# Kernel optimization log

Hardware: AMD Instinct MI355X
Metric: run time of the kernel (lower is better)

## Reference

```python
import jax, jax.numpy as jnp
import numpy as np

N, E, G, T, H, ED, IN_D, OUT_D = 50000, 1600000, 64, 5, 64, 9, 10, 3
EPS = 1e-6

def _seg_mean(vals, seg, num):
    s = jax.ops.segment_sum(vals, seg, num_segments=num)
    c = jax.ops.segment_sum(jnp.ones((vals.shape[0],), vals.dtype), seg, num_segments=num)
    return s / jnp.maximum(c, 1.0)[:, None], c

def per_graph_edge_norm(edge_attr, edge_graph, num_graphs):
    # standardize each edge-feature column per graph (zero-shot transfer trick)
    mu, _ = _seg_mean(edge_attr, edge_graph, num_graphs)
    sq, _ = _seg_mean(edge_attr * edge_attr, edge_graph, num_graphs)
    var = jnp.maximum(sq - mu * mu, 0.0)
    std = jnp.sqrt(var)
    return (edge_attr - mu[edge_graph]) / (std[edge_graph] + EPS)

def setup_inputs() -> dict:
    key = jax.random.key(0)
    ks = jax.random.split(key, 24)
    s = 0.05  # weight scale to keep ReLU chains stable
    inp = {
        'x': jax.random.normal(ks[0], (N, IN_D), jnp.float32),
        'edge_index': jax.random.randint(ks[1], (2, E), 0, N),
        'edge_attr': jax.random.normal(ks[2], (E, ED), jnp.float32),
        'batch': jnp.sort(jax.random.randint(ks[3], (N,), 0, G)),
        'lift_W1': jax.random.normal(ks[4], (IN_D, H), jnp.float32) * s,
        'lift_b1': jnp.zeros((H,), jnp.float32),
        'lift_W2': jax.random.normal(ks[5], (H, H), jnp.float32) * s,
        'lift_b2': jnp.zeros((H,), jnp.float32),
        'Wself': jax.random.normal(ks[6], (T, H, H), jnp.float32) * s,
        'bself': jnp.zeros((T, H), jnp.float32),
        'msg_W0': jax.random.normal(ks[7], (T, H + ED, H), jnp.float32) * s,
        'msg_b0': jnp.zeros((T, H), jnp.float32),
        'msg_W1': jax.random.normal(ks[8], (T, H, H), jnp.float32) * s,
        'msg_b1': jnp.zeros((T, H), jnp.float32),
        'msg_W2': jax.random.normal(ks[9], (T, H, H), jnp.float32) * s,
        'msg_b2': jnp.zeros((T, H), jnp.float32),
        'gate_W': jax.random.normal(ks[10], (T, 1, H), jnp.float32) * s,
        'gate_b': jnp.zeros((T, H), jnp.float32),
        'proj_W1': jax.random.normal(ks[11], (H, H), jnp.float32) * s,
        'proj_b1': jnp.zeros((H,), jnp.float32),
        'proj_W2': jax.random.normal(ks[12], (H, OUT_D), jnp.float32) * s,
        'proj_b2': jnp.zeros((OUT_D,), jnp.float32),
    }
    return inp

def _gno(x, edge_index, edge_attr, batch,
         lift_W1, lift_b1, lift_W2, lift_b2,
         Wself, bself, msg_W0, msg_b0, msg_W1, msg_b1, msg_W2, msg_b2,
         gate_W, gate_b, proj_W1, proj_b1, proj_W2, proj_b2):
    src, dst = edge_index[0], edge_index[1]
    edge_graph = batch[src]
    ea = per_graph_edge_norm(edge_attr, edge_graph, G)  # cols 0:9 == all cols
    log_diag_y = x[:, 4:5]                               # [N,1]
    v0 = jax.nn.relu(x @ lift_W1 + lift_b1) @ lift_W2 + lift_b2  # lift
    v = v0
    for t in range(T):
        # gather -> per-edge MLP -> scatter-mean (AdmittanceKernelLayer)
        h = jnp.concatenate([v[src], ea], axis=-1)              # [E, H+ED]
        h = jax.nn.relu(h @ msg_W0[t] + msg_b0[t])
        h = jax.nn.relu(h @ msg_W1[t] + msg_b1[t])
        m = h @ msg_W2[t] + msg_b2[t]                           # [E, H]
        agg, _ = _seg_mean(m, dst, N)                           # mean aggregation
        gate = jax.nn.sigmoid(log_diag_y @ gate_W[t] + gate_b[t])  # [N,H]
        v = jax.nn.relu(v @ Wself[t] + bself[t] + agg + v0) * gate
        # dropout inactive at inference
    out = jax.nn.relu(v @ proj_W1 + proj_b1) @ proj_W2 + proj_b2  # project
    return out

def reference(x, edge_index, edge_attr, batch,
              lift_W1, lift_b1, lift_W2, lift_b2,
              Wself, bself, msg_W0, msg_b0, msg_W1, msg_b1, msg_W2, msg_b2,
              gate_W, gate_b, proj_W1, proj_b1, proj_W2, proj_b2):
    return _gno(x, edge_index, edge_attr, batch,
                lift_W1, lift_b1, lift_W2, lift_b2,
                Wself, bself, msg_W0, msg_b0, msg_W1, msg_b1, msg_W2, msg_b2,
                gate_W, gate_b, proj_W1, proj_b1, proj_W2, proj_b2)
```

## Files before the change

### kernel.cpp

```cpp
#include <hip/hip_runtime.h>
#include <math.h>

#define NN 50000
#define NE 1600000
#define NG 64
#define NT 5
#define NH 64
#define NED 9
#define NIN 10
#define NOUT 3
#define EPSF 1e-6f
#define NSUB (NE / 16)
#define STATS_BLKS 2048
#define STATS_SLICE (2 * NG * NED + NG)

typedef __attribute__((ext_vector_type(8))) short s8v;
typedef __attribute__((ext_vector_type(4))) short s4v;
typedef __attribute__((ext_vector_type(4))) float f32x4;

__device__ __forceinline__ unsigned short f2bf(float f) {
    union { float f; unsigned int u; } v; v.f = f;
    unsigned int r = v.u + 0x7FFFu + ((v.u >> 16) & 1u);
    return (unsigned short)(r >> 16);
}
__device__ __forceinline__ float bf2f(unsigned short b) {
    union { unsigned int u; float f; } v; v.u = ((unsigned int)b) << 16;
    return v.f;
}

__global__ __launch_bounds__(256) void stats_kernel(
    const int* __restrict__ ei, const float* __restrict__ ea,
    const int* __restrict__ batch,
    float* __restrict__ blockAcc, int* __restrict__ ecnt) {
    __shared__ float lsum[NG * NED];
    __shared__ float lsq[NG * NED];
    __shared__ float lcnt[NG];
    for (int i = threadIdx.x; i < NG * NED; i += blockDim.x) { lsum[i] = 0.f; lsq[i] = 0.f; }
    for (int i = threadIdx.x; i < NG; i += blockDim.x) lcnt[i] = 0.f;
    __syncthreads();
    const int TOT = NE * NED;
    int stride = gridDim.x * blockDim.x;
    for (int i = blockIdx.x * blockDim.x + threadIdx.x; i < TOT; i += stride) {
        int e = (int)(((unsigned long long)i * 0x1C71C71D) >> 32);
        int d = i - e * NED;
        float a = ea[i];
        int g = batch[ei[e]];
        atomicAdd(&lsum[g * NED + d], a);
        atomicAdd(&lsq[g * NED + d], a * a);
        if (d == 0) {
            atomicAdd(&lcnt[g], 1.0f);
            atomicAdd(&ecnt[ei[NE + e]], 1);
        }
    }
    __syncthreads();
    float* dst = blockAcc + (size_t)blockIdx.x * STATS_SLICE;
    for (int i = threadIdx.x; i < NG * NED; i += blockDim.x) {
        dst[i] = lsum[i];
        dst[NG * NED + i] = lsq[i];
    }
    for (int i = threadIdx.x; i < NG; i += blockDim.x) dst[2 * NG * NED + i] = lcnt[i];
}

__global__ void stats_merge(const float* __restrict__ blockAcc,
                            float* __restrict__ ssum, float* __restrict__ ssq,
                            float* __restrict__ scnt) {
    int i = blockIdx.x * 256 + threadIdx.x;
    if (i >= STATS_SLICE) return;
    float a = 0.f;
    for (int b = 0; b < STATS_BLKS; ++b) a += blockAcc[(size_t)b * STATS_SLICE + i];
    if (i < NG * NED) ssum[i] = a;
    else if (i < 2 * NG * NED) ssq[i - NG * NED] = a;
    else scnt[i - 2 * NG * NED] = a;
}

__global__ void stats_fin(const float* __restrict__ ssum, const float* __restrict__ ssq,
                          const float* __restrict__ scnt,
                          float* __restrict__ mu, float* __restrict__ rstd) {
    int i = blockIdx.x * blockDim.x + threadIdx.x;
    if (i >= NG * NED) return;
    int g = i / NED;
    float c = fmaxf(scnt[g], 1.0f);
    float m = ssum[i] / c;
    float q = ssq[i] / c;
    float var = fmaxf(q - m * m, 0.f);
    mu[i] = m;
    rstd[i] = 1.0f / (sqrtf(var) + EPSF);
}

__global__ void scan1_kernel(const int* __restrict__ ecnt, int* __restrict__ partial) {
    __shared__ int sm[256];
    int i = blockIdx.x * 256 + threadIdx.x;
    sm[threadIdx.x] = (i < NN) ? ecnt[i] : 0;
    __syncthreads();
    for (int off = 128; off; off >>= 1) {
        if (threadIdx.x < off) sm[threadIdx.x] += sm[threadIdx.x + off];
        __syncthreads();
    }
    if (threadIdx.x == 0) partial[blockIdx.x] = sm[0];
}
__global__ void scan2_kernel(int* __restrict__ partial, int nb) {
    __shared__ int sm[256];
    int t = threadIdx.x;
    sm[t] = (t < nb) ? partial[t] : 0;
    __syncthreads();
    for (int off = 1; off < 256; off <<= 1) {
        int v = (t >= off) ? sm[t - off] : 0;
        __syncthreads();
        sm[t] += v;
        __syncthreads();
    }
    if (t < nb) partial[t] = (t ? sm[t - 1] : 0);
}
__global__ void scan3_kernel(const int* __restrict__ ecnt, const int* __restrict__ partial,
                             int* __restrict__ offs) {
    __shared__ int sm[256];
    int b = blockIdx.x, t = threadIdx.x, i = b * 256 + t;
    int x = (i < NN) ? ecnt[i] : 0;
    sm[t] = x;
    __syncthreads();
    for (int off = 1; off < 256; off <<= 1) {
        int v = (t >= off) ? sm[t - off] : 0;
        __syncthreads();
        sm[t] += v;
        __syncthreads();
    }
    if (i < NN) offs[i] = sm[t] - x + partial[b];
}

__global__ void permute_kernel(const int* __restrict__ ei, const int* __restrict__ offs,
                               int* __restrict__ cursor, int* __restrict__ perm) {
    int stride = gridDim.x * blockDim.x;
    for (int e = blockIdx.x * blockDim.x + threadIdx.x; e < NE; e += stride) {
        int d = ei[NE + e];
        int pos = offs[d] + atomicAdd(&cursor[d], 1);
        perm[pos] = e;
    }
}

__global__ void pack_kernel(const int* __restrict__ perm, const int* __restrict__ ei,
                            const float* __restrict__ ea, const int* __restrict__ batch,
                            const float* __restrict__ mu, const float* __restrict__ rstd,
                            int* __restrict__ srcPerm, int* __restrict__ dstPerm,
                            unsigned short* __restrict__ eaN) {
    int stride = gridDim.x * blockDim.x;
    for (int p = blockIdx.x * blockDim.x + threadIdx.x; p < NE; p += stride) {
        int e = perm[p];
        int s = ei[e], d = ei[NE + e];
        int g = batch[s];
        srcPerm[p] = s;
        dstPerm[p] = d;
#pragma unroll
        for (int k = 0; k < NED; ++k) {
            float val = (ea[(size_t)e * NED + k] - mu[g * NED + k]) * rstd[g * NED + k];
            eaN[(size_t)k * NE + p] = f2bf(val);
        }
    }
}

__global__ __launch_bounds__(256) void lift_kernel(
    const float* __restrict__ x,
    const float* __restrict__ W1, const float* __restrict__ b1,
    const float* __restrict__ W2, const float* __restrict__ b2,
    float* __restrict__ v0, float* __restrict__ v, float* __restrict__ ldy) {
    __shared__ float sW1[NIN * NH];
    __shared__ __align__(16) float sW2[NH][NH];
    __shared__ float sb1[NH], sb2[NH];
    for (int i = threadIdx.x; i < NIN * NH; i += blockDim.x) sW1[i] = W1[i];
    for (int i = threadIdx.x; i < NH * NH; i += blockDim.x) {
        int k = i >> 6, j = i & 63;
        sW2[j][k] = W2[i];
    }
    for (int i = threadIdx.x; i < NH; i += blockDim.x) { sb1[i] = b1[i]; sb2[i] = b2[i]; }
    __syncthreads();
    int stride = gridDim.x * blockDim.x;
    for (int n = blockIdx.x * blockDim.x + threadIdx.x; n < NN; n += stride) {
        float xr[NIN];
#pragma unroll
        for (int k = 0; k < NIN; ++k) xr[k] = x[(size_t)n * NIN + k];
        ldy[n] = xr[4];
        float h[NH];
#pragma unroll
        for (int j = 0; j < NH; ++j) {
            float acc = sb1[j];
#pragma unroll
            for (int k = 0; k < NIN; ++k) acc += xr[k] * sW1[k * NH + j];
            h[j] = fmaxf(acc, 0.f);
        }
#pragma unroll
        for (int j = 0; j < NH; ++j) {
            float acc = sb2[j];
#pragma unroll
            for (int k = 0; k < NH; k += 4) {
                float4 w = *(const float4*)&sW2[j][k];
                acc += h[k] * w.x + h[k + 1] * w.y + h[k + 2] * w.z + h[k + 3] * w.w;
            }
            v0[(size_t)n * NH + j] = acc;
            v[(size_t)n * NH + j] = acc;
        }
    }
}

__device__ __forceinline__ void gemm_acc68(const float* __restrict__ Ab,
                                           const float* __restrict__ Wb,
                                           int K, int te, int tj, float acc[4][4]) {
#pragma unroll 4
    for (int k = 0; k < K; ++k) {
        float4 a = *(const float4*)(Ab + k * 68 + (te << 2));
        float4 b = *(const float4*)(Wb + (k << 6) + (tj << 2));
        acc[0][0] = fmaf(a.x, b.x, acc[0][0]);
        acc[0][1] = fmaf(a.x, b.y, acc[0][1]);
        acc[0][2] = fmaf(a.x, b.z, acc[0][2]);
        acc[0][3] = fmaf(a.x, b.w, acc[0][3]);
        acc[1][0] = fmaf(a.y, b.x, acc[1][0]);
        acc[1][1] = fmaf(a.y, b.y, acc[1][1]);
        acc[1][2] = fmaf(a.y, b.z, acc[1][2]);
        acc[1][3] = fmaf(a.y, b.w, acc[1][3]);
        acc[2][0] = fmaf(a.z, b.x, acc[2][0]);
        acc[2][1] = fmaf(a.z, b.y, acc[2][1]);
        acc[2][2] = fmaf(a.z, b.z, acc[2][2]);
        acc[2][3] = fmaf(a.z, b.w, acc[2][3]);
        acc[3][0] = fmaf(a.w, b.x, acc[3][0]);
        acc[3][1] = fmaf(a.w, b.y, acc[3][1]);
        acc[3][2] = fmaf(a.w, b.z, acc[3][2]);
        acc[3][3] = fmaf(a.w, b.w, acc[3][3]);
    }
}

__global__ __launch_bounds__(256, 4) void u_kernel(
    const float* __restrict__ v, const float* __restrict__ W0v,
    const float* __restrict__ b0, unsigned short* __restrict__ Ubf) {
    __shared__ __align__(16) float Vt[64][68];
    __shared__ __align__(16) float sW[64][64];
    __shared__ float sb[64];
    const int tid = threadIdx.x;
    const int base = blockIdx.x * 64;
    const int te = tid >> 4, tj = tid & 15;

    {
        int r = tid >> 2;
        int kb = (tid & 3) << 4;
        int n = base + r;
        const float4* vrow = (const float4*)(v + (size_t)n * NH + kb);
#pragma unroll
        for (int q = 0; q < 4; ++q) {
            float4 f = (n < NN) ? vrow[q] : make_float4(0.f, 0.f, 0.f, 0.f);
            int k = kb + q * 4;
            Vt[k + 0][r] = f.x; Vt[k + 1][r] = f.y; Vt[k + 2][r] = f.z; Vt[k + 3][r] = f.w;
        }
    }
    for (int i4 = tid; i4 < 64 * 16; i4 += 256) {
        int k = i4 >> 4, c4 = i4 & 15;
        *(float4*)&sW[k][c4 * 4] = *(const float4*)(W0v + (size_t)k * 64 + c4 * 4);
    }
    if (tid < 64) sb[tid] = b0[tid];
    __syncthreads();

    float acc[4][4];
    {
        float b0_ = sb[tj * 4 + 0], b1_ = sb[tj * 4 + 1], b2_ = sb[tj * 4 + 2], b3_ = sb[tj * 4 + 3];
#pragma unroll
        for (int ee = 0; ee < 4; ++ee) { acc[ee][0] = b0_; acc[ee][1] = b1_; acc[ee][2] = b2_; acc[ee][3] = b3_; }
    }
    gemm_acc68(&Vt[0][0], &sW[0][0], 64, te, tj, acc);

#pragma unroll
    for (int ee = 0; ee < 4; ++ee) {
        int n = base + te * 4 + ee;
        if (n < NN) {
            s4v p;
            p[0] = (short)f2bf(acc[ee][0]);
            p[1] = (short)f2bf(acc[ee][1]);
            p[2] = (short)f2bf(acc[ee][2]);
            p[3] = (short)f2bf(acc[ee][3]);
            *(s4v*)&Ubf[(size_t)n * NH + tj * 4] = p;
        }
    }
}

__global__ __launch_bounds__(256, 4) void edge4_kernel(
    const int* __restrict__ srcPerm, const int* __restrict__ dstPerm,
    const unsigned short* __restrict__ eaN,
    const float* __restrict__ W0e, const float* __restrict__ W1, const float* __restrict__ b1,
    const unsigned short* __restrict__ Ubf, float* __restrict__ nodesum) {
    __shared__ __align__(16) float sWe[NED][64];
    __shared__ __align__(16) short W1frag[8][64][8];
    __shared__ __align__(16) short h0bf[4][16 * 64];
    __shared__ __align__(16) float h1s[4][16 * 64];
    __shared__ int sDstS[4][16];

    const int tid = threadIdx.x;
    const int lane = tid & 63, w = tid >> 6;
    const int l15 = lane & 15, l4 = lane >> 4;

    for (int i4 = tid; i4 < NED * 16; i4 += 256) {
        int k = i4 >> 4, c4 = i4 & 15;
        *(float4*)&sWe[k][c4 * 4] = *(const float4*)(W0e + (size_t)k * 64 + c4 * 4);
    }
    for (int idx = tid; idx < 2 * 4 * 64; idx += 256) {
        int kc = idx >> 8, c = (idx >> 6) & 3, ln = idx & 63;
        int fl15 = ln & 15, fl4 = ln >> 4;
        int col = 16 * c + fl15;
        s8v frag;
#pragma unroll
        for (int j = 0; j < 8; ++j) {
            int k = kc * 32 + fl4 * 8 + j;
            frag[j] = (short)f2bf(W1[(size_t)k * 64 + col]);
        }
        *(s8v*)&W1frag[kc * 4 + c][ln][0] = frag;
    }
    float b1r[4];
#pragma unroll
    for (int c = 0; c < 4; ++c) b1r[c] = b1[16 * c + l15];
    __syncthreads();

    short* myh0 = h0bf[w];
    float* myh1 = h1s[w];
    int*   myd  = sDstS[w];
    const int gw = blockIdx.x * 4 + w;
    const int nw = gridDim.x * 4;

    for (int st = gw; st < NSUB; st += nw) {
        const int e16 = st * 16;
        if (lane < 16) myd[lane] = dstPerm[e16 + lane];

        int4 s4 = *(const int4*)(srcPerm + e16 + 4 * l4);
        ushort4 eu[NED];
#pragma unroll
        for (int d = 0; d < NED; ++d)
            eu[d] = *(const ushort4*)(eaN + (size_t)d * NE + e16 + 4 * l4);

        float acc0[4][4];
        {
            const int* sp = (const int*)&s4;
#pragma unroll
            for (int ee = 0; ee < 4; ++ee) {
                s4v u4 = *(const s4v*)(Ubf + (size_t)sp[ee] * NH + 4 * l15);
                acc0[ee][0] = bf2f((unsigned short)u4[0]);
                acc0[ee][1] = bf2f((unsigned short)u4[1]);
                acc0[ee][2] = bf2f((unsigned short)u4[2]);
                acc0[ee][3] = bf2f((unsigned short)u4[3]);
            }
        }
#pragma unroll
        for (int d = 0; d < NED; ++d) {
            float4 wv = *(const float4*)&sWe[d][4 * l15];
            float a0 = bf2f((unsigned short)eu[d].x), a1 = bf2f((unsigned short)eu[d].y);
            float a2 = bf2f((unsigned short)eu[d].z), a3 = bf2f((unsigned short)eu[d].w);
            acc0[0][0] = fmaf(a0, wv.x, acc0[0][0]); acc0[0][1] = fmaf(a0, wv.y, acc0[0][1]);
            acc0[0][2] = fmaf(a0, wv.z, acc0[0][2]); acc0[0][3] = fmaf(a0, wv.w, acc0[0][3]);
            acc0[1][0] = fmaf(a1, wv.x, acc0[1][0]); acc0[1][1] = fmaf(a1, wv.y, acc0[1][1]);
            acc0[1][2] = fmaf(a1, wv.z, acc0[1][2]); acc0[1][3] = fmaf(a1, wv.w, acc0[1][3]);
            acc0[2][0] = fmaf(a2, wv.x, acc0[2][0]); acc0[2][1] = fmaf(a2, wv.y, acc0[2][1]);
            acc0[2][2] = fmaf(a2, wv.z, acc0[2][2]); acc0[2][3] = fmaf(a2, wv.w, acc0[2][3]);
            acc0[3][0] = fmaf(a3, wv.x, acc0[3][0]); acc0[3][1] = fmaf(a3, wv.y, acc0[3][1]);
            acc0[3][2] = fmaf(a3, wv.z, acc0[3][2]); acc0[3][3] = fmaf(a3, wv.w, acc0[3][3]);
        }

#pragma unroll
        for (int ee = 0; ee < 4; ++ee) {
            int row = 4 * l4 + ee;
            s4v p;
            p[0] = (short)f2bf(fmaxf(acc0[ee][0], 0.f));
            p[1] = (short)f2bf(fmaxf(acc0[ee][1], 0.f));
            p[2] = (short)f2bf(fmaxf(acc0[ee][2], 0.f));
            p[3] = (short)f2bf(fmaxf(acc0[ee][3], 0.f));
            *(s4v*)((char*)myh0 + row * 128 + ((l15 * 8) ^ ((row & 7) << 4))) = p;
        }

        f32x4 acc[4];
#pragma unroll
        for (int c = 0; c < 4; ++c) {
            float b = b1r[c];
            acc[c][0] = b; acc[c][1] = b; acc[c][2] = b; acc[c][3] = b;
        }
        {
            const char* abase = (const char*)myh0 + l15 * 128;
            const int aswz = (l15 & 7) << 4;
#pragma unroll
            for (int kc = 0; kc < 2; ++kc) {
                s8v af = *(const s8v*)(abase + ((l4 * 16 + kc * 64) ^ aswz));
#pragma unroll
                for (int c = 0; c < 4; ++c) {
                    s8v bf = *(const s8v*)&W1frag[kc * 4 + c][lane][0];
                    acc[c] = __builtin_amdgcn_mfma_f32_16x16x32_bf16(af, bf, acc[c], 0, 0, 0);
                }
            }
        }

        int dFirst = myd[0];
        int dLast = myd[15];
        if (dFirst == dLast) {
#pragma unroll
            for (int c = 0; c < 4; ++c) {
                float vs = fmaxf(acc[c][0], 0.f) + fmaxf(acc[c][1], 0.f) +
                           fmaxf(acc[c][2], 0.f) + fmaxf(acc[c][3], 0.f);
                vs += __shfl_xor(vs, 16);
                vs += __shfl_xor(vs, 32);
                if (l4 == 0)
                    atomicAdd(&nodesum[(size_t)dFirst * NH + 16 * c + l15], vs);
            }
        } else {
#pragma unroll
            for (int r = 0; r < 4; ++r) {
                int row = 4 * l4 + r;
#pragma unroll
                for (int c = 0; c < 4; ++c)
                    myh1[row * 64 + ((16 * c + l15) ^ (l4 * 8))] = fmaxf(acc[c][r], 0.f);
            }
            int cur = dFirst;
            float a = myh1[lane];
#pragma unroll
            for (int i = 1; i < 16; ++i) {
                int dn = myd[i];
                float hv = myh1[i * 64 + (lane ^ ((i >> 2) * 8))];
                if (dn != cur) {
                    atomicAdd(&nodesum[(size_t)cur * NH + lane], a);
                    cur = dn;
                    a = hv;
                } else {
                    a += hv;
                }
            }
            atomicAdd(&nodesum[(size_t)cur * NH + lane], a);
        }
    }
}

__global__ __launch_bounds__(256, 2) void update3_kernel(
    const float* __restrict__ Wself, const float* __restrict__ bself,
    const float* __restrict__ W2, const float* __restrict__ b2,
    const float* __restrict__ gWt, const float* __restrict__ gbt,
    const float* __restrict__ v0, const float* __restrict__ ldy,
    const int* __restrict__ ecnt, float* __restrict__ nodesum,
    float* __restrict__ v) {
    __shared__ __align__(16) float Vt[64][68];
    __shared__ __align__(16) float St[64][68];
    __shared__ __align__(16) float sWs[64][64];
    __shared__ __align__(16) float sW2[64][64];
    __shared__ float sbs[64], sb2[64], sgw[64], sgb[64];
    const int tid = threadIdx.x;
    const int base = blockIdx.x * 64;
    const int te = tid >> 4, tj = tid & 15;

    {
        int r = tid >> 2;
        int kb = (tid & 3) << 4;
        int n = base + r;
        const float4* vrow = (const float4*)(v + (size_t)n * NH + kb);
        float4* srow = (float4*)(nodesum + (size_t)n * NH + kb);
        const float4 z4 = make_float4(0.f, 0.f, 0.f, 0.f);
#pragma unroll
        for (int q = 0; q < 4; ++q) {
            float4 f = (n < NN) ? vrow[q] : z4;
            float4 g = (n < NN) ? srow[q] : z4;
            if (n < NN) srow[q] = z4;
            int k = kb + q * 4;
            Vt[k + 0][r] = f.x; Vt[k + 1][r] = f.y; Vt[k + 2][r] = f.z; Vt[k + 3][r] = f.w;
            St[k + 0][r] = g.x; St[k + 1][r] = g.y; St[k + 2][r] = g.z; St[k + 3][r] = g.w;
        }
    }
    for (int i4 = tid; i4 < 64 * 16; i4 += 256) {
        int k = i4 >> 4, c4 = i4 & 15;
        *(float4*)&sWs[k][c4 * 4] = *(const float4*)(Wself + (size_t)k * 64 + c4 * 4);
        *(float4*)&sW2[k][c4 * 4] = *(const float4*)(W2 + (size_t)k * 64 + c4 * 4);
    }
    if (tid < 64) { sbs[tid] = bself[tid]; sb2[tid] = b2[tid]; sgw[tid] = gWt[tid]; sgb[tid] = gbt[tid]; }
    __syncthreads();

    float acc1[4][4], acc2[4][4];
    {
        float b0_ = sbs[tj * 4 + 0], b1_ = sbs[tj * 4 + 1], b2_ = sbs[tj * 4 + 2], b3_ = sbs[tj * 4 + 3];
#pragma unroll
        for (int ee = 0; ee < 4; ++ee) {
            acc1[ee][0] = b0_; acc1[ee][1] = b1_; acc1[ee][2] = b2_; acc1[ee][3] = b3_;
            acc2[ee][0] = 0.f; acc2[ee][1] = 0.f; acc2[ee][2] = 0.f; acc2[ee][3] = 0.f;
        }
    }
    gemm_acc68(&Vt[0][0], &sWs[0][0], 64, te, tj, acc1);
    gemm_acc68(&St[0][0], &sW2[0][0], 64, te, tj, acc2);

    float gw0 = sgw[tj * 4 + 0], gw1 = sgw[tj * 4 + 1], gw2 = sgw[tj * 4 + 2], gw3 = sgw[tj * 4 + 3];
    float gb0 = sgb[tj * 4 + 0], gb1 = sgb[tj * 4 + 1], gb2 = sgb[tj * 4 + 2], gb3 = sgb[tj * 4 + 3];
    float bb0 = sb2[tj * 4 + 0], bb1 = sb2[tj * 4 + 1], bb2 = sb2[tj * 4 + 2], bb3 = sb2[tj * 4 + 3];
#pragma unroll
    for (int ee = 0; ee < 4; ++ee) {
        int n = base + te * 4 + ee;
        if (n >= NN) continue;
        float cnt = (float)ecnt[n];
        float has = (cnt > 0.5f) ? 1.f : 0.f;
        float dninv = has / fmaxf(cnt, 1.f);
        float ld = ldy[n];
        float4 v0r = *(const float4*)&v0[(size_t)n * NH + tj * 4];
        float z0 = acc1[ee][0] + acc2[ee][0] * dninv + bb0 * has + v0r.x;
        float z1 = acc1[ee][1] + acc2[ee][1] * dninv + bb1 * has + v0r.y;
        float z2 = acc1[ee][2] + acc2[ee][2] * dninv + bb2 * has + v0r.z;
        float z3 = acc1[ee][3] + acc2[ee][3] * dninv + bb3 * has + v0r.w;
        float g0 = 1.f / (1.f + expf(-(ld * gw0 + gb0)));
        float g1 = 1.f / (1.f + expf(-(ld * gw1 + gb1)));
        float g2 = 1.f / (1.f + expf(-(ld * gw2 + gb2)));
        float g3 = 1.f / (1.f + expf(-(ld * gw3 + gb3)));
        *(float4*)&v[(size_t)n * NH + tj * 4] =
            make_float4(fmaxf(z0, 0.f) * g0, fmaxf(z1, 0.f) * g1,
                        fmaxf(z2, 0.f) * g2, fmaxf(z3, 0.f) * g3);
    }
}

__global__ __launch_bounds__(256) void proj_kernel(
    const float* __restrict__ v,
    const float* __restrict__ pW1, const float* __restrict__ pb1,
    const float* __restrict__ pW2, const float* __restrict__ pb2,
    float* __restrict__ out) {
    __shared__ __align__(16) float sW1[NH][NH];
    __shared__ float sb1[NH];
    __shared__ float sW2[NH * NOUT];
    __shared__ float sb2[NOUT];
    for (int i = threadIdx.x; i < NH * NH; i += blockDim.x) {
        int k = i >> 6, j = i & 63;
        sW1[j][k] = pW1[i];
    }
    for (int i = threadIdx.x; i < NH; i += blockDim.x) sb1[i] = pb1[i];
    for (int i = threadIdx.x; i < NH * NOUT; i += blockDim.x) sW2[i] = pW2[i];
    for (int i = threadIdx.x; i < NOUT; i += blockDim.x) sb2[i] = pb2[i];
    __syncthreads();
    int stride = gridDim.x * blockDim.x;
    for (int n = blockIdx.x * blockDim.x + threadIdx.x; n < NN; n += stride) {
        float vr[NH];
        const float4* vp = (const float4*)(v + (size_t)n * NH);
#pragma unroll
        for (int q = 0; q < NH / 4; ++q) {
            float4 f = vp[q];
            vr[4 * q + 0] = f.x; vr[4 * q + 1] = f.y; vr[4 * q + 2] = f.z; vr[4 * q + 3] = f.w;
        }
        float o0 = sb2[0], o1 = sb2[1], o2 = sb2[2];
#pragma unroll
        for (int j = 0; j < NH; ++j) {
            float acc = sb1[j];
#pragma unroll
            for (int k = 0; k < NH; k += 4) {
                float4 w = *(const float4*)&sW1[j][k];
                acc += vr[k] * w.x + vr[k + 1] * w.y + vr[k + 2] * w.z + vr[k + 3] * w.w;
            }
            float h = fmaxf(acc, 0.f);
            o0 += h * sW2[j * NOUT + 0];
            o1 += h * sW2[j * NOUT + 1];
            o2 += h * sW2[j * NOUT + 2];
        }
        out[(size_t)n * NOUT + 0] = o0;
        out[(size_t)n * NOUT + 1] = o1;
        out[(size_t)n * NOUT + 2] = o2;
    }
}

extern "C" void kernel_launch(void* const* d_in, const int* in_sizes, int n_in,
                              void* d_out, int out_size, void* d_ws, size_t ws_size,
                              hipStream_t stream) {
    (void)in_sizes; (void)n_in; (void)out_size; (void)ws_size;
    const float* x     = (const float*)d_in[0];
    const int*   ei    = (const int*)d_in[1];
    const float* ea    = (const float*)d_in[2];
    const int*   batch = (const int*)d_in[3];
    const float* lW1   = (const float*)d_in[4];
    const float* lb1   = (const float*)d_in[5];
    const float* lW2   = (const float*)d_in[6];
    const float* lb2   = (const float*)d_in[7];
    const float* Wself = (const float*)d_in[8];
    const float* bself = (const float*)d_in[9];
    const float* mW0   = (const float*)d_in[10];
    const float* mb0   = (const float*)d_in[11];
    const float* mW1   = (const float*)d_in[12];
    const float* mb1   = (const float*)d_in[13];
    const float* mW2   = (const float*)d_in[14];
    const float* mb2   = (const float*)d_in[15];
    const float* gW    = (const float*)d_in[16];
    const float* gb    = (const float*)d_in[17];
    const float* pW1   = (const float*)d_in[18];
    const float* pb1   = (const float*)d_in[19];
    const float* pW2   = (const float*)d_in[20];
    const float* pb2   = (const float*)d_in[21];
    float* out = (float*)d_out;
    float* ws  = (float*)d_ws;

    float* nodesum = ws;
    float* v0   = nodesum + (size_t)NN * NH;
    float* v    = v0 + (size_t)NN * NH;
    unsigned short* Ubf = (unsigned short*)(v + (size_t)NN * NH);
    float* ldy  = (float*)Ubf + (size_t)NN * NH;
    float* mu   = ldy + NN;
    float* rstd = mu + NG * NED;
    float* ssum = rstd + NG * NED;
    float* ssq  = ssum + NG * NED;
    float* scnt = ssq + NG * NED;
    int*   ecnt   = (int*)(scnt + NG);
    int*   cursor = ecnt + NN;
    int*   offs    = cursor + NN;
    int*   partial = offs + NN;
    int*   srcPerm = partial + 256;
    int*   dstPerm = srcPerm + NE;
    unsigned short* eaN = (unsigned short*)(dstPerm + NE);
    float* statsPart = (float*)(eaN + (size_t)NED * NE);
    int*   perm = (int*)nodesum;

    const int NBLK = (NN + 63) / 64;
    const int SBLK = (NN + 255) / 256;

    hipMemsetAsync(ecnt, 0, (size_t)2 * NN * sizeof(int), stream);

    stats_kernel<<<STATS_BLKS, 256, 0, stream>>>(ei, ea, batch, statsPart, ecnt);
    stats_merge<<<(STATS_SLICE + 255) / 256, 256, 0, stream>>>(statsPart, ssum, ssq, scnt);
    stats_fin<<<3, 256, 0, stream>>>(ssum, ssq, scnt, mu, rstd);
    scan1_kernel<<<SBLK, 256, 0, stream>>>(ecnt, partial);
    scan2_kernel<<<1, 256, 0, stream>>>(partial, SBLK);
    scan3_kernel<<<SBLK, 256, 0, stream>>>(ecnt, partial, offs);
    permute_kernel<<<2048, 256, 0, stream>>>(ei, offs, cursor, perm);
    pack_kernel<<<2048, 256, 0, stream>>>(perm, ei, ea, batch, mu, rstd, srcPerm, dstPerm, eaN);
    lift_kernel<<<200, 256, 0, stream>>>(x, lW1, lb1, lW2, lb2, v0, v, ldy);

    hipMemsetAsync(nodesum, 0, (size_t)NN * NH * sizeof(float), stream);

    for (int t = 0; t < NT; ++t) {
        const float* W0t = mW0 + (size_t)t * (NH + NED) * NH;
        u_kernel<<<NBLK, 256, 0, stream>>>(v, W0t, mb0 + (size_t)t * NH, Ubf);
        edge4_kernel<<<1024, 256, 0, stream>>>(
            srcPerm, dstPerm, eaN,
            W0t + (size_t)NH * NH,
            mW1 + (size_t)t * NH * NH, mb1 + (size_t)t * NH,
            Ubf, nodesum);
        update3_kernel<<<NBLK, 256, 0, stream>>>(
            Wself + (size_t)t * NH * NH, bself + (size_t)t * NH,
            mW2 + (size_t)t * NH * NH, mb2 + (size_t)t * NH,
            gW + (size_t)t * NH, gb + (size_t)t * NH,
            v0, ldy, ecnt, nodesum, v);
    }
    proj_kernel<<<200, 256, 0, stream>>>(v, pW1, pb1, pW2, pb2, out);
}
```

Measured before the change: 1.452 ms.

## Sort edges by graph to compute per-graph edge stats with wave reductions

Replaces the per-element shared-atomic statistics pass with a three-stage path: histogram edges by graph id (storing a byte graph id per edge), bucket them into a graph-sorted permutation, then read edge attributes in that order. Because most wavefronts then see a single graph, each wavefront sums its values with shuffles and issues only a few global atomics, and the block-partials merge kernel is removed. Pack also reuses the cached graph id instead of a dependent batch[src] gather. The cost is extra kernels, a gathered (non-coalesced) read of edge_attr through the permutation, and float atomic ordering that makes the sums nondeterministic.

```diff
diff --git a/kernel.cpp b/kernel.cpp
--- a/kernel.cpp
+++ b/kernel.cpp
@@ -11,8 +11,8 @@
 #define NOUT 3
 #define EPSF 1e-6f
 #define NSUB (NE / 16)
-#define STATS_BLKS 2048
-#define STATS_SLICE (2 * NG * NED + NG)
+#define GP_CHUNK 2000
+#define GP_GRID (NE / GP_CHUNK)
 
 typedef __attribute__((ext_vector_type(8))) short s8v;
 typedef __attribute__((ext_vector_type(4))) short s4v;
@@ -28,58 +28,99 @@
     return v.f;
 }
 
-__global__ __launch_bounds__(256) void stats_kernel(
-    const int* __restrict__ ei, const float* __restrict__ ea,
-    const int* __restrict__ batch,
-    float* __restrict__ blockAcc, int* __restrict__ ecnt) {
-    __shared__ float lsum[NG * NED];
-    __shared__ float lsq[NG * NED];
-    __shared__ float lcnt[NG];
-    for (int i = threadIdx.x; i < NG * NED; i += blockDim.x) { lsum[i] = 0.f; lsq[i] = 0.f; }
-    for (int i = threadIdx.x; i < NG; i += blockDim.x) lcnt[i] = 0.f;
-    __syncthreads();
-    const int TOT = NE * NED;
+__global__ __launch_bounds__(256) void ghist_kernel(
+    const int* __restrict__ ei, const int* __restrict__ batch,
+    unsigned char* __restrict__ gId, int* __restrict__ gtot, int* __restrict__ ecnt) {
+    __shared__ int lh[NG];
+    for (int i = threadIdx.x; i < NG; i += 256) lh[i] = 0;
+    __syncthreads();
     int stride = gridDim.x * blockDim.x;
-    for (int i = blockIdx.x * blockDim.x + threadIdx.x; i < TOT; i += stride) {
-        int e = (int)(((unsigned long long)i * 0x1C71C71D) >> 32);
-        int d = i - e * NED;
-        float a = ea[i];
+    for (int e = blockIdx.x * blockDim.x + threadIdx.x; e < NE; e += stride) {
         int g = batch[ei[e]];
-        atomicAdd(&lsum[g * NED + d], a);
-        atomicAdd(&lsq[g * NED + d], a * a);
-        if (d == 0) {
-            atomicAdd(&lcnt[g], 1.0f);
-            atomicAdd(&ecnt[ei[NE + e]], 1);
-        }
-    }
-    __syncthreads();
-    float* dst = blockAcc + (size_t)blockIdx.x * STATS_SLICE;
-    for (int i = threadIdx.x; i < NG * NED; i += blockDim.x) {
-        dst[i] = lsum[i];
-        dst[NG * NED + i] = lsq[i];
-    }
-    for (int i = threadIdx.x; i < NG; i += blockDim.x) dst[2 * NG * NED + i] = lcnt[i];
-}
-
-__global__ void stats_merge(const float* __restrict__ blockAcc,
-                            float* __restrict__ ssum, float* __restrict__ ssq,
-                            float* __restrict__ scnt) {
-    int i = blockIdx.x * 256 + threadIdx.x;
-    if (i >= STATS_SLICE) return;
-    float a = 0.f;
-    for (int b = 0; b < STATS_BLKS; ++b) a += blockAcc[(size_t)b * STATS_SLICE + i];
-    if (i < NG * NED) ssum[i] = a;
-    else if (i < 2 * NG * NED) ssq[i - NG * NED] = a;
-    else scnt[i - 2 * NG * NED] = a;
+        gId[e] = (unsigned char)g;
+        atomicAdd(&lh[g], 1);
+        atomicAdd(&ecnt[ei[NE + e]], 1);
+    }
+    __syncthreads();
+    for (int i = threadIdx.x; i < NG; i += 256) atomicAdd(&gtot[i], lh[i]);
+}
+
+__global__ void gscan_kernel(const int* __restrict__ gtot, int* __restrict__ gbase) {
+    if (threadIdx.x == 0) {
+        int acc = 0;
+        for (int g = 0; g < NG; ++g) { gbase[g] = acc; acc += gtot[g]; }
+    }
+}
+
+__global__ __launch_bounds__(256) void gpermute_kernel(
+    const unsigned char* __restrict__ gId, const int* __restrict__ gbase,
+    int* __restrict__ gcursor, int* __restrict__ gperm) {
+    __shared__ int lh[NG], sbase[NG], lcur[NG];
+    const int b0 = blockIdx.x * GP_CHUNK;
+    for (int i = threadIdx.x; i < NG; i += 256) { lh[i] = 0; lcur[i] = 0; }
+    __syncthreads();
+    for (int i = threadIdx.x; i < GP_CHUNK; i += 256)
+        atomicAdd(&lh[gId[b0 + i]], 1);
+    __syncthreads();
+    if (threadIdx.x < NG)
+        sbase[threadIdx.x] = gbase[threadIdx.x] +
+                             atomicAdd(&gcursor[threadIdx.x], lh[threadIdx.x]);
+    __syncthreads();
+    for (int i = threadIdx.x; i < GP_CHUNK; i += 256) {
+        int e = b0 + i;
+        int g = gId[e];
+        int pos = sbase[g] + atomicAdd(&lcur[g], 1);
+        gperm[pos] = (g << 24) | e;
+    }
+}
+
+__global__ __launch_bounds__(256) void statsg_kernel(
+    const int* __restrict__ gperm, const float* __restrict__ ea,
+    float* __restrict__ ssum, float* __restrict__ ssq) {
+    int stride = gridDim.x * blockDim.x;
+    int lane = threadIdx.x & 63;
+    for (int p = blockIdx.x * blockDim.x + threadIdx.x; p < NE; p += stride) {
+        int pe = gperm[p];
+        int g = pe >> 24;
+        int e = pe & 0xFFFFFF;
+        float a[NED], q[NED];
+        const float* er = ea + (size_t)e * NED;
+#pragma unroll
+        for (int d = 0; d < NED; ++d) { a[d] = er[d]; q[d] = a[d] * a[d]; }
+        int g0 = __builtin_amdgcn_readfirstlane(g);
+        if (__all(g == g0)) {
+#pragma unroll
+            for (int off = 32; off; off >>= 1) {
+#pragma unroll
+                for (int d = 0; d < NED; ++d) {
+                    a[d] += __shfl_xor(a[d], off);
+                    q[d] += __shfl_xor(q[d], off);
+                }
+            }
+            if (lane == 0) {
+#pragma unroll
+                for (int d = 0; d < NED; ++d) atomicAdd(&ssum[g0 * NED + d], a[d]);
+            } else if (lane == 1) {
+#pragma unroll
+                for (int d = 0; d < NED; ++d) atomicAdd(&ssq[g0 * NED + d], q[d]);
+            }
+        } else {
+#pragma unroll
+            for (int d = 0; d < NED; ++d) {
+                atomicAdd(&ssum[g * NED + d], a[d]);
+                atomicAdd(&ssq[g * NED + d], q[d]);
+            }
+        }
+    }
 }
 
 __global__ void stats_fin(const float* __restrict__ ssum, const float* __restrict__ ssq,
-                          const float* __restrict__ scnt,
+                          const int* __restrict__ gtot,
                           float* __restrict__ mu, float* __restrict__ rstd) {
     int i = blockIdx.x * blockDim.x + threadIdx.x;
     if (i >= NG * NED) return;
     int g = i / NED;
-    float c = fmaxf(scnt[g], 1.0f);
+    float c = fmaxf((float)gtot[g], 1.0f);
     float m = ssum[i] / c;
     float q = ssq[i] / c;
     float var = fmaxf(q - m * m, 0.f);
@@ -138,7 +179,7 @@
 }
 
 __global__ void pack_kernel(const int* __restrict__ perm, const int* __restrict__ ei,
-                            const float* __restrict__ ea, const int* __restrict__ batch,
+                            const float* __restrict__ ea, const unsigned char* __restrict__ gId,
                             const float* __restrict__ mu, const float* __restrict__ rstd,
                             int* __restrict__ srcPerm, int* __restrict__ dstPerm,
                             unsigned short* __restrict__ eaN) {
@@ -146,7 +187,7 @@
     for (int p = blockIdx.x * blockDim.x + threadIdx.x; p < NE; p += stride) {
         int e = perm[p];
         int s = ei[e], d = ei[NE + e];
-        int g = batch[s];
+        int g = gId[e];
         srcPerm[p] = s;
         dstPerm[p] = d;
 #pragma unroll
@@ -589,30 +630,35 @@
     float* rstd = mu + NG * NED;
     float* ssum = rstd + NG * NED;
     float* ssq  = ssum + NG * NED;
-    float* scnt = ssq + NG * NED;
-    int*   ecnt   = (int*)(scnt + NG);
-    int*   cursor = ecnt + NN;
-    int*   offs    = cursor + NN;
+    int*   ecnt    = (int*)(ssq + NG * NED);
+    int*   cursor  = ecnt + NN;
+    int*   gtot    = cursor + NN;
+    int*   gcursor = gtot + NG;
+    int*   gbase   = gcursor + NG;
+    int*   offs    = gbase + NG;
     int*   partial = offs + NN;
     int*   srcPerm = partial + 256;
     int*   dstPerm = srcPerm + NE;
-    unsigned short* eaN = (unsigned short*)(dstPerm + NE);
-    float* statsPart = (float*)(eaN + (size_t)NED * NE);
+    int*   gperm   = dstPerm + NE;
+    unsigned short* eaN = (unsigned short*)(gperm + NE);
+    unsigned char*  gId = (unsigned char*)(eaN + (size_t)NED * NE);
     int*   perm = (int*)nodesum;
 
     const int NBLK = (NN + 63) / 64;
     const int SBLK = (NN + 255) / 256;
 
-    hipMemsetAsync(ecnt, 0, (size_t)2 * NN * sizeof(int), stream);
-
-    stats_kernel<<<STATS_BLKS, 256, 0, stream>>>(ei, ea, batch, statsPart, ecnt);
-    stats_merge<<<(STATS_SLICE + 255) / 256, 256, 0, stream>>>(statsPart, ssum, ssq, scnt);
-    stats_fin<<<3, 256, 0, stream>>>(ssum, ssq, scnt, mu, rstd);
+    hipMemsetAsync(ssum, 0, ((size_t)(2 * NG * NED) + 2 * NN + 2 * NG) * sizeof(float), stream);
+
+    ghist_kernel<<<2048, 256, 0, stream>>>(ei, batch, gId, gtot, ecnt);
+    gscan_kernel<<<1, 64, 0, stream>>>(gtot, gbase);
+    gpermute_kernel<<<GP_GRID, 256, 0, stream>>>(gId, gbase, gcursor, gperm);
+    statsg_kernel<<<2048, 256, 0, stream>>>(gperm, ea, ssum, ssq);
+    stats_fin<<<3, 256, 0, stream>>>(ssum, ssq, gtot, mu, rstd);
     scan1_kernel<<<SBLK, 256, 0, stream>>>(ecnt, partial);
     scan2_kernel<<<1, 256, 0, stream>>>(partial, SBLK);
     scan3_kernel<<<SBLK, 256, 0, stream>>>(ecnt, partial, offs);
     permute_kernel<<<2048, 256, 0, stream>>>(ei, offs, cursor, perm);
-    pack_kernel<<<2048, 256, 0, stream>>>(perm, ei, ea, batch, mu, rstd, srcPerm, dstPerm, eaN);
+    pack_kernel<<<2048, 256, 0, stream>>>(perm, ei, ea, gId, mu, rstd, srcPerm, dstPerm, eaN);
     lift_kernel<<<200, 256, 0, stream>>>(x, lW1, lb1, lW2, lb2, v0, v, ldy);
 
     hipMemsetAsync(nodesum, 0, (size_t)NN * NH * sizeof(float), stream);
```

Result: slower. 1.746 ms (+20.3%).
